# Kernel tuning notes

Measured on AMD Instinct MI355X. Metric: run time of the kernel, lower is better.

The kernel has to match this reference:

```python
import jax, jax.numpy as jnp
import numpy as np

B = 2_000_000
ND = 3

def _skew(v):
    # v: [B,3] -> [B,3,3] skew-symmetric matrix
    z = jnp.zeros_like(v[..., 0])
    r0 = jnp.stack([z, -v[..., 2], v[..., 1]], axis=-1)
    r1 = jnp.stack([v[..., 2], z, -v[..., 0]], axis=-1)
    r2 = jnp.stack([-v[..., 1], v[..., 0], z], axis=-1)
    return jnp.stack([r0, r1, r2], axis=-2)

def _rotmat(v):
    # Closed-form expm of skew(v) (Rodrigues). Mathematically identical to tf.linalg.expm.
    th2 = jnp.sum(v * v, axis=-1)                      # [B]
    th = jnp.sqrt(th2)
    small = th < 1e-6
    th_s = jnp.where(small, 1.0, th)
    th2_s = jnp.where(small, 1.0, th2)
    a = jnp.where(small, 1.0, jnp.sin(th) / th_s)      # sin(t)/t
    b = jnp.where(small, 0.5, (1.0 - jnp.cos(th)) / th2_s)  # (1-cos t)/t^2
    K = _skew(v)                                       # [B,3,3]
    I = jnp.eye(ND, dtype=v.dtype)
    return I + a[:, None, None] * K + b[:, None, None] * jnp.matmul(K, K)

def setup_inputs() -> dict:
    key = jax.random.key(0)
    k1, k2, k3, k4 = jax.random.split(key, 4)
    trans = jax.random.normal(k1, (B, ND), dtype=jnp.float32)
    rotat = jax.random.normal(k2, (B, ND), dtype=jnp.float32)
    scal_dir = jax.random.normal(k3, (B, ND), dtype=jnp.float32)
    scal = jax.random.normal(k4, (B, ND), dtype=jnp.float32)
    return {"trans": trans, "rotat": rotat, "scal_dir": scal_dir, "scal": scal}

def reference(trans, rotat, scal_dir, scal):
    R = _rotmat(rotat)          # [B,3,3] rotation
    U = _rotmat(scal_dir)       # [B,3,3] scaling direction
    D = jnp.exp(scal)           # expm(diag(s)) == diag(exp(s)), [B,3]
    # U @ diag(D) @ U^T, then R @ (.)
    Ut = jnp.swapaxes(U, -1, -2)
    M = jnp.matmul(U, D[:, :, None] * Ut)   # diag(D) @ U^T broadcast as row-scaling
    M = jnp.matmul(R, M)
    return jnp.concatenate([M, trans[:, :, None]], axis=2)  # [B,3,4]
```

## Files before the change

### kernel.cpp

```cpp
#include <hip/hip_runtime.h>
#include <math.h>

__device__ __forceinline__ void rodrigues(const float v0, const float v1, const float v2,
                                          float R[9]) {
    float th2 = v0 * v0 + v1 * v1 + v2 * v2;
    float th  = sqrtf(th2);
    float s, c;
    sincosf(th, &s, &c);
    bool  sm = th < 1e-6f;
    float a  = sm ? 1.0f : s / th;
    float b  = sm ? 0.5f : (1.0f - c) / th2;
    float cc = 1.0f - b * th2;
    R[0] = cc + b * v0 * v0;  R[1] = b * v0 * v1 - a * v2;  R[2] = b * v0 * v2 + a * v1;
    R[3] = b * v0 * v1 + a * v2;  R[4] = cc + b * v1 * v1;  R[5] = b * v1 * v2 - a * v0;
    R[6] = b * v0 * v2 - a * v1;  R[7] = b * v1 * v2 + a * v0;  R[8] = cc + b * v2 * v2;
}

__global__ __launch_bounds__(256) void aff_kernel(
    const float4* __restrict__ trans,
    const float4* __restrict__ rotat,
    const float4* __restrict__ sdir,
    const float4* __restrict__ scal,
    float4* __restrict__ out,
    int nq)
{
    int t = blockIdx.x * blockDim.x + threadIdx.x;
    if (t >= nq) return;

    float4 tr4[3], ro4[3], sd4[3], sc4[3];
#pragma unroll
    for (int i = 0; i < 3; ++i) {
        tr4[i] = trans[3 * t + i];
        ro4[i] = rotat[3 * t + i];
        sd4[i] = sdir [3 * t + i];
        sc4[i] = scal [3 * t + i];
    }
    float tr[12], ro[12], sd[12], sc[12];
#pragma unroll
    for (int i = 0; i < 3; ++i) {
        tr[4*i+0]=tr4[i].x; tr[4*i+1]=tr4[i].y; tr[4*i+2]=tr4[i].z; tr[4*i+3]=tr4[i].w;
        ro[4*i+0]=ro4[i].x; ro[4*i+1]=ro4[i].y; ro[4*i+2]=ro4[i].z; ro[4*i+3]=ro4[i].w;
        sd[4*i+0]=sd4[i].x; sd[4*i+1]=sd4[i].y; sd[4*i+2]=sd4[i].z; sd[4*i+3]=sd4[i].w;
        sc[4*i+0]=sc4[i].x; sc[4*i+1]=sc4[i].y; sc[4*i+2]=sc4[i].z; sc[4*i+3]=sc4[i].w;
    }

#pragma unroll
    for (int e = 0; e < 4; ++e) {
        float R[9], U[9];
        rodrigues(ro[3*e+0], ro[3*e+1], ro[3*e+2], R);
        rodrigues(sd[3*e+0], sd[3*e+1], sd[3*e+2], U);
        float d0 = expf(sc[3*e+0]);
        float d1 = expf(sc[3*e+1]);
        float d2 = expf(sc[3*e+2]);

        float W[9];
#pragma unroll
        for (int i = 0; i < 3; ++i) {
            W[3*i+0] = U[3*i+0] * d0;
            W[3*i+1] = U[3*i+1] * d1;
            W[3*i+2] = U[3*i+2] * d2;
        }
        float S[9];
#pragma unroll
        for (int i = 0; i < 3; ++i)
#pragma unroll
            for (int j = 0; j < 3; ++j)
                S[3*i+j] = W[3*i+0]*U[3*j+0] + W[3*i+1]*U[3*j+1] + W[3*i+2]*U[3*j+2];
        float M[9];
#pragma unroll
        for (int i = 0; i < 3; ++i)
#pragma unroll
            for (int j = 0; j < 3; ++j)
                M[3*i+j] = R[3*i+0]*S[0+j] + R[3*i+1]*S[3+j] + R[3*i+2]*S[6+j];

        int base = 12 * t + 3 * e;
        out[base + 0] = make_float4(M[0], M[1], M[2], tr[3*e+0]);
        out[base + 1] = make_float4(M[3], M[4], M[5], tr[3*e+1]);
        out[base + 2] = make_float4(M[6], M[7], M[8], tr[3*e+2]);
    }
}

extern "C" void kernel_launch(void* const* d_in, const int* in_sizes, int n_in,
                              void* d_out, int out_size, void* d_ws, size_t ws_size,
                              hipStream_t stream) {
    const float4* tr = (const float4*)d_in[0];
    const float4* ro = (const float4*)d_in[1];
    const float4* sd = (const float4*)d_in[2];
    const float4* sc = (const float4*)d_in[3];
    float4* out = (float4*)d_out;

    int Btot = in_sizes[0] / 3;
    int nq   = Btot / 4;
    const int threads = 256;
    int blocks = (nq + threads - 1) / threads;
    aff_kernel<<<blocks, threads, 0, stream>>>(tr, ro, sd, sc, out, nq);
}
```

Measured before the change: 215.3 us.

## Stage inputs and outputs through LDS for coalesced access, one element per thread

Switches from one thread handling four elements with strided float4 loads and stores to one element per thread. Each block now loads its inputs coalesced into shared memory and writes results into a shared output buffer. The block then stores that buffer to global memory with fully coalesced float4 writes. This targets the uncoalesced 48-byte-stride access of the old scheme, at the cost of two block barriers, LDS traffic, and four times as many threads and blocks.

```diff
diff --git a/kernel.cpp b/kernel.cpp
--- a/kernel.cpp
+++ b/kernel.cpp
@@ -1,8 +1,9 @@
 #include <hip/hip_runtime.h>
 #include <math.h>
 
-__device__ __forceinline__ void rodrigues(const float v0, const float v1, const float v2,
-                                          float R[9]) {
+#define TPB 256
+
+__device__ __forceinline__ void rodrigues(float v0, float v1, float v2, float R[9]) {
     float th2 = v0 * v0 + v1 * v1 + v2 * v2;
     float th  = sqrtf(th2);
     float s, c;
@@ -11,47 +12,49 @@
     float a  = sm ? 1.0f : s / th;
     float b  = sm ? 0.5f : (1.0f - c) / th2;
     float cc = 1.0f - b * th2;
-    R[0] = cc + b * v0 * v0;  R[1] = b * v0 * v1 - a * v2;  R[2] = b * v0 * v2 + a * v1;
-    R[3] = b * v0 * v1 + a * v2;  R[4] = cc + b * v1 * v1;  R[5] = b * v1 * v2 - a * v0;
+    R[0] = cc + b * v0 * v0;      R[1] = b * v0 * v1 - a * v2;  R[2] = b * v0 * v2 + a * v1;
+    R[3] = b * v0 * v1 + a * v2;  R[4] = cc + b * v1 * v1;      R[5] = b * v1 * v2 - a * v0;
     R[6] = b * v0 * v2 - a * v1;  R[7] = b * v1 * v2 + a * v0;  R[8] = cc + b * v2 * v2;
 }
 
-__global__ __launch_bounds__(256) void aff_kernel(
+__global__ __launch_bounds__(TPB) void aff_kernel(
     const float4* __restrict__ trans,
     const float4* __restrict__ rotat,
     const float4* __restrict__ sdir,
     const float4* __restrict__ scal,
     float4* __restrict__ out,
-    int nq)
+    int B)
 {
-    int t = blockIdx.x * blockDim.x + threadIdx.x;
-    if (t >= nq) return;
+    __shared__ float s_in[4][TPB * 3];
+    __shared__ float s_out[TPB * 12];
 
-    float4 tr4[3], ro4[3], sd4[3], sc4[3];
-#pragma unroll
-    for (int i = 0; i < 3; ++i) {
-        tr4[i] = trans[3 * t + i];
-        ro4[i] = rotat[3 * t + i];
-        sd4[i] = sdir [3 * t + i];
-        sc4[i] = scal [3 * t + i];
+    const int tid  = threadIdx.x;
+    const int base = blockIdx.x * TPB;
+    const int n    = min(TPB, B - base);
+    const int nf4  = (n * 3) >> 2;
+
+    if (tid < nf4) {
+        const int gbase = (base * 3) >> 2;
+        float4 a = trans[gbase + tid];
+        float4 b = rotat[gbase + tid];
+        float4 c = sdir [gbase + tid];
+        float4 d = scal [gbase + tid];
+        ((float4*)&s_in[0][0])[tid] = a;
+        ((float4*)&s_in[1][0])[tid] = b;
+        ((float4*)&s_in[2][0])[tid] = c;
+        ((float4*)&s_in[3][0])[tid] = d;
     }
-    float tr[12], ro[12], sd[12], sc[12];
-#pragma unroll
-    for (int i = 0; i < 3; ++i) {
-        tr[4*i+0]=tr4[i].x; tr[4*i+1]=tr4[i].y; tr[4*i+2]=tr4[i].z; tr[4*i+3]=tr4[i].w;
-        ro[4*i+0]=ro4[i].x; ro[4*i+1]=ro4[i].y; ro[4*i+2]=ro4[i].z; ro[4*i+3]=ro4[i].w;
-        sd[4*i+0]=sd4[i].x; sd[4*i+1]=sd4[i].y; sd[4*i+2]=sd4[i].z; sd[4*i+3]=sd4[i].w;
-        sc[4*i+0]=sc4[i].x; sc[4*i+1]=sc4[i].y; sc[4*i+2]=sc4[i].z; sc[4*i+3]=sc4[i].w;
-    }
+    __syncthreads();
 
-#pragma unroll
-    for (int e = 0; e < 4; ++e) {
+    if (tid < n) {
+        float t0 = s_in[0][3*tid+0], t1 = s_in[0][3*tid+1], t2 = s_in[0][3*tid+2];
+
         float R[9], U[9];
-        rodrigues(ro[3*e+0], ro[3*e+1], ro[3*e+2], R);
-        rodrigues(sd[3*e+0], sd[3*e+1], sd[3*e+2], U);
-        float d0 = expf(sc[3*e+0]);
-        float d1 = expf(sc[3*e+1]);
-        float d2 = expf(sc[3*e+2]);
+        rodrigues(s_in[1][3*tid+0], s_in[1][3*tid+1], s_in[1][3*tid+2], R);
+        rodrigues(s_in[2][3*tid+0], s_in[2][3*tid+1], s_in[2][3*tid+2], U);
+        float d0 = expf(s_in[3][3*tid+0]);
+        float d1 = expf(s_in[3][3*tid+1]);
+        float d2 = expf(s_in[3][3*tid+2]);
 
         float W[9];
 #pragma unroll
@@ -73,10 +76,20 @@
             for (int j = 0; j < 3; ++j)
                 M[3*i+j] = R[3*i+0]*S[0+j] + R[3*i+1]*S[3+j] + R[3*i+2]*S[6+j];
 
-        int base = 12 * t + 3 * e;
-        out[base + 0] = make_float4(M[0], M[1], M[2], tr[3*e+0]);
-        out[base + 1] = make_float4(M[3], M[4], M[5], tr[3*e+1]);
-        out[base + 2] = make_float4(M[6], M[7], M[8], tr[3*e+2]);
+        float4* so = (float4*)s_out;
+        so[3*tid+0] = make_float4(M[0], M[1], M[2], t0);
+        so[3*tid+1] = make_float4(M[3], M[4], M[5], t1);
+        so[3*tid+2] = make_float4(M[6], M[7], M[8], t2);
+    }
+    __syncthreads();
+
+    const int nq = n * 3;
+    const float4* so = (const float4*)s_out;
+    const int ob = base * 3;
+#pragma unroll
+    for (int p = 0; p < 3; ++p) {
+        int idx = p * TPB + tid;
+        if (idx < nq) out[ob + idx] = so[idx];
     }
 }
 
@@ -89,9 +102,7 @@
     const float4* sc = (const float4*)d_in[3];
     float4* out = (float4*)d_out;
 
-    int Btot = in_sizes[0] / 3;
-    int nq   = Btot / 4;
-    const int threads = 256;
-    int blocks = (nq + threads - 1) / threads;
-    aff_kernel<<<blocks, threads, 0, stream>>>(tr, ro, sd, sc, out, nq);
+    int B = in_sizes[0] / 3;
+    int blocks = (B + TPB - 1) / TPB;
+    aff_kernel<<<blocks, TPB, 0, stream>>>(tr, ro, sd, sc, out, B);
 }
```

New measurement: 176.2 us. 1.22x faster.
